# Kernel optimization log

Measured on AMD Instinct MI355X. Metric: run time of the kernel, lower is better.

The kernel has to match this reference:

```python
import jax, jax.numpy as jnp
import numpy as np

B, S, D, H, HD = 2, 2048, 2048, 16, 128  # batch, seq, embed, heads, head_dim


def setup_inputs() -> dict:
    key = jax.random.key(0)
    k0, k1, k2 = jax.random.split(key, 3)
    hidden_states = jax.random.normal(k0, (B, S, D), dtype=jnp.float32)
    # fused QKV projection: [D, H*HD + 2*HD] (multi-query: single shared K and V head)
    W_attn = jax.random.normal(k1, (D, H * HD + 2 * HD), dtype=jnp.float32) * 0.02
    b_attn = jnp.zeros((H * HD + 2 * HD,), dtype=jnp.float32)
    W_proj = jax.random.normal(k2, (D, D), dtype=jnp.float32) * 0.02
    b_proj = jnp.zeros((D,), dtype=jnp.float32)
    # causal mask, broadcastable to (B, Q, H, K); True = attend
    attention_mask = jnp.tril(jnp.ones((S, S), dtype=bool))[None, :, None, :]
    return {
        "hidden_states": hidden_states,
        "W_attn": W_attn,
        "b_attn": b_attn,
        "W_proj": W_proj,
        "b_proj": b_proj,
        "attention_mask": attention_mask,
    }


def reference(hidden_states, W_attn, b_attn, W_proj, b_proj, attention_mask):
    # fused QKV, then split into Q (H heads) and shared K/V (multi-query)
    qkv = hidden_states @ W_attn + b_attn          # (B, S, H*HD + 2*HD)
    q = qkv[..., : H * HD].reshape(B, S, H, HD)    # (B, Q, H, hd)
    key_t = qkv[..., H * HD : H * HD + HD]         # (B, K, hd) shared K head
    value = qkv[..., H * HD + HD :]                # (B, K, hd) shared V head

    # dtype == softmax_dtype (fp32) -> upcast=False, unscale=1
    scale_factor = 1.0 / (HD ** 0.5)               # scale_attn_weights
    attn_weights = jnp.einsum("bqhd,bkd->bqhk", q, key_t) * scale_factor
    mask_value = jnp.finfo(jnp.float32).min
    attn_weights = jnp.where(attention_mask, attn_weights, mask_value)
    attn_weights = jax.nn.softmax(attn_weights, axis=-1)

    attn_output = jnp.einsum("bqhk,bkd->bqhd", attn_weights, value)
    attn_output = attn_output.reshape(B, S, H * HD)
    return attn_output @ W_proj + b_proj           # (B, S, D)
```

## Files before the change

### kernel.cpp

```cpp
#include <hip/hip_runtime.h>
#include <math.h>

constexpr int cB  = 2;
constexpr int cS  = 2048;
constexpr int cD  = 2048;
constexpr int cH  = 16;
constexpr int cHD = 128;
constexpr int cNQKV = cH * cHD + 2 * cHD;

typedef __attribute__((ext_vector_type(8))) short bf16x8;
typedef __attribute__((ext_vector_type(4))) float f32x4;

__device__ __forceinline__ short f2bf(float f) {
    union { float f; unsigned u; } v; v.f = f;
    unsigned r = (v.u + 0x7FFFu + ((v.u >> 16) & 1u)) >> 16;
    return (short)r;
}

typedef __attribute__((address_space(3))) void lds_t;
typedef const __attribute__((address_space(1))) void gbl_t;
__device__ __forceinline__ void gld16(const void* g, void* l) {
    __builtin_amdgcn_global_load_lds((gbl_t*)g, (lds_t*)l, 16, 0, 0);
}

__global__ __launch_bounds__(256) void conv_bf16(
    const float* __restrict__ src, short* __restrict__ dst)
{
    size_t i = ((size_t)blockIdx.x * 256 + threadIdx.x) * 8;
    float4 a = *(const float4*)(src + i);
    float4 b = *(const float4*)(src + i + 4);
    bf16x8 o;
    o[0] = f2bf(a.x); o[1] = f2bf(a.y); o[2] = f2bf(a.z); o[3] = f2bf(a.w);
    o[4] = f2bf(b.x); o[5] = f2bf(b.y); o[6] = f2bf(b.z); o[7] = f2bf(b.w);
    *(bf16x8*)(dst + i) = o;
}

__global__ __launch_bounds__(256) void transpose_bf16(
    const float* __restrict__ src, short* __restrict__ dst, int K, int N)
{
    __shared__ short t[32][33];
    const int n0 = blockIdx.x * 32, k0 = blockIdx.y * 32;
    const int x = threadIdx.x & 31, y = threadIdx.x >> 5;
#pragma unroll
    for (int i = 0; i < 4; ++i)
        t[y + 8 * i][x] = f2bf(src[(size_t)(k0 + y + 8 * i) * N + n0 + x]);
    __syncthreads();
#pragma unroll
    for (int i = 0; i < 4; ++i)
        dst[(size_t)(n0 + y + 8 * i) * K + k0 + x] = t[x][y + 8 * i];
}

template<bool BF16_OUT>
__global__ __launch_bounds__(256) void gemm_mfma(
    const short* __restrict__ A, const short* __restrict__ Bt,
    const float* __restrict__ bias, void* __restrict__ Cout,
    int M, int N, int K, float qscale, int qcols)
{
    __shared__ short As[128 * 32];
    __shared__ short Bs[128 * 32];

    const int tid = threadIdx.x;
    const int lane = tid & 63, n16 = lane & 15, quad = lane >> 4;
    const int wave = tid >> 6, wm = wave >> 1, wn = wave & 1;
    const int m0 = blockIdx.y * 128, n0 = blockIdx.x * 128;

    f32x4 acc[4][4];
#pragma unroll
    for (int i = 0; i < 4; ++i)
#pragma unroll
        for (int j = 0; j < 4; ++j) acc[i][j] = 0.0f;

    const int s0 = tid, s1 = tid + 256;
    const short* Ag0 = A  + (size_t)(m0 + (s0 >> 2)) * K + (s0 & 3) * 8;
    const short* Ag1 = A  + (size_t)(m0 + (s1 >> 2)) * K + (s1 & 3) * 8;
    const short* Bg0 = Bt + (size_t)(n0 + (s0 >> 2)) * K + (s0 & 3) * 8;
    const short* Bg1 = Bt + (size_t)(n0 + (s1 >> 2)) * K + (s1 & 3) * 8;

    for (int k0 = 0; k0 < K; k0 += 32) {
        gld16(Ag0 + k0, &As[s0 * 8]);
        gld16(Ag1 + k0, &As[s1 * 8]);
        gld16(Bg0 + k0, &Bs[s0 * 8]);
        gld16(Bg1 + k0, &Bs[s1 * 8]);
        __syncthreads();
        bf16x8 af[4], bfr[4];
#pragma unroll
        for (int mt = 0; mt < 4; ++mt)
            af[mt] = *(const bf16x8*)&As[(wm * 64 + mt * 16 + n16) * 32 + quad * 8];
#pragma unroll
        for (int nt = 0; nt < 4; ++nt)
            bfr[nt] = *(const bf16x8*)&Bs[(wn * 64 + nt * 16 + n16) * 32 + quad * 8];
#pragma unroll
        for (int mt = 0; mt < 4; ++mt)
#pragma unroll
            for (int nt = 0; nt < 4; ++nt)
                acc[mt][nt] = __builtin_amdgcn_mfma_f32_16x16x32_bf16(
                    af[mt], bfr[nt], acc[mt][nt], 0, 0, 0);
        __syncthreads();
    }

#pragma unroll
    for (int nt = 0; nt < 4; ++nt) {
        const int col = n0 + wn * 64 + nt * 16 + n16;
        const float bv = bias[col];
        const float sc = (col < qcols) ? qscale : 1.0f;
#pragma unroll
        for (int mt = 0; mt < 4; ++mt)
#pragma unroll
            for (int r = 0; r < 4; ++r) {
                const int row = m0 + wm * 64 + mt * 16 + quad * 4 + r;
                const float v = (acc[mt][nt][r] + bv) * sc;
                if (BF16_OUT) ((short*)Cout)[(size_t)row * N + col] = f2bf(v);
                else          ((float*)Cout)[(size_t)row * N + col] = v;
            }
    }
}

__global__ __launch_bounds__(256) void prep_v(
    const short* __restrict__ qkvb, short* __restrict__ Vt)
{
    const int b  = blockIdx.y;
    const int k0 = blockIdx.x * 64;
    const int t  = threadIdx.x;
#pragma unroll
    for (int i = 0; i < 32; ++i) {
        int idx = i * 256 + t;
        int hd = idx >> 6, key = idx & 63;
        Vt[((size_t)b * cHD + hd) * cS + k0 + key] =
            qkvb[((size_t)(b * cS + k0 + key)) * cNQKV + cH * cHD + cHD + hd];
    }
}

__global__ __launch_bounds__(256) void attn_mfma(
    const short* __restrict__ qkvb, const short* __restrict__ Vt,
    short* __restrict__ out)
{
    const int tid  = threadIdx.x;
    const int wave = tid >> 6;
    const int lane = tid & 63;
    const int n16  = lane & 15;
    const int quad = lane >> 4;
    const int h  = blockIdx.y;
    const int b  = blockIdx.z;

    __shared__ __align__(16) short Ks[2][8192];
    __shared__ __align__(16) short Vs[2][8192];
    __shared__ __align__(16) short Ps[4][16][72];

    const int part = lane & 3;
    const int krow = lane >> 2;

    const short* kglob = qkvb + (size_t)b * cS * cNQKV + cH * cHD;
    const short* vbase = Vt + (size_t)b * cHD * cS;

    int cur = 0;

    auto stage = [&](int buf, int k0) {
        const short* kr = kglob + (size_t)(k0 + wave * 16 + krow) * cNQKV + part * 8;
#pragma unroll
        for (int j = 0; j < 4; ++j)
            gld16(kr + j * 32, &Ks[buf][(j * 4 + wave) * 512]);
#pragma unroll
        for (int j = 0; j < 4; ++j) {
            const int idx = j * 4 + wave;
            const int c2 = idx >> 3;
            const int hd = (idx & 7) * 16 + krow;
            gld16(vbase + (size_t)hd * cS + k0 + c2 * 32 + part * 8,
                  &Vs[buf][idx * 512]);
        }
    };

#pragma unroll 1
    for (int seg = 0; seg < 2; ++seg) {
        const int qt = seg ? (int)blockIdx.x : 31 - (int)blockIdx.x;
        const int q0 = qt * 64 + wave * 16;
        const int nkt = qt + 1;

        bf16x8 qf[4];
        {
            const short* qbase = qkvb + ((size_t)(b * cS) + q0 + n16) * cNQKV
                               + h * cHD + quad * 8;
#pragma unroll
            for (int ch = 0; ch < 4; ++ch) qf[ch] = *(const bf16x8*)(qbase + ch * 32);
        }

        f32x4 oc[8];
#pragma unroll
        for (int on = 0; on < 8; ++on) oc[on] = 0.0f;
        float lp[4] = {0.0f, 0.0f, 0.0f, 0.0f};

        __syncthreads();
        stage(cur, 0);

#pragma unroll 1
        for (int kt = 0; kt < nkt; ++kt) {
            const int k0 = kt * 64;
            __syncthreads();
            if (kt + 1 < nkt) stage(cur ^ 1, k0 + 64);

            f32x4 sc[4];
#pragma unroll
            for (int nt = 0; nt < 4; ++nt) sc[nt] = 0.0f;
            __builtin_amdgcn_s_setprio(1);
#pragma unroll
            for (int nt = 0; nt < 4; ++nt) {
#pragma unroll
                for (int ch = 0; ch < 4; ++ch) {
                    bf16x8 kf = *(const bf16x8*)&Ks[cur][(ch * 64 + nt * 16 + n16) * 32 + quad * 8];
                    sc[nt] = __builtin_amdgcn_mfma_f32_16x16x32_bf16(qf[ch], kf, sc[nt], 0, 0, 0);
                }
            }
            __builtin_amdgcn_s_setprio(0);

            if (kt == nkt - 1) {
#pragma unroll
                for (int nt = 0; nt < 4; ++nt)
#pragma unroll
                    for (int r = 0; r < 4; ++r) {
                        int row = q0 + quad * 4 + r;
                        int col = k0 + nt * 16 + n16;
                        if (col > row) sc[nt][r] = -1e30f;
                    }
            }

#pragma unroll
            for (int r = 0; r < 4; ++r)
#pragma unroll
                for (int nt = 0; nt < 4; ++nt) {
                    float p = __expf(sc[nt][r]);
                    lp[r] += p;
                    Ps[wave][quad * 4 + r][nt * 16 + n16] = f2bf(p);
                }

            bf16x8 pf0 = *(const bf16x8*)&Ps[wave][n16][quad * 8];
            bf16x8 pf1 = *(const bf16x8*)&Ps[wave][n16][32 + quad * 8];

            __builtin_amdgcn_s_setprio(1);
#pragma unroll
            for (int on = 0; on < 8; ++on) {
                bf16x8 vf0 = *(const bf16x8*)&Vs[cur][(on * 16 + n16) * 32 + quad * 8];
                bf16x8 vf1 = *(const bf16x8*)&Vs[cur][(128 * 32) + (on * 16 + n16) * 32 + quad * 8];
                oc[on] = __builtin_amdgcn_mfma_f32_16x16x32_bf16(pf0, vf0, oc[on], 0, 0, 0);
                oc[on] = __builtin_amdgcn_mfma_f32_16x16x32_bf16(pf1, vf1, oc[on], 0, 0, 0);
            }
            __builtin_amdgcn_s_setprio(0);

            cur ^= 1;
        }

        float inv[4];
#pragma unroll
        for (int r = 0; r < 4; ++r) {
            float t = lp[r];
            t += __shfl_xor(t, 1);
            t += __shfl_xor(t, 2);
            t += __shfl_xor(t, 4);
            t += __shfl_xor(t, 8);
            inv[r] = 1.0f / t;
        }
        short* obase = out + ((size_t)(b * cS) + q0) * cD + h * cHD;
#pragma unroll
        for (int on = 0; on < 8; ++on)
#pragma unroll
            for (int r = 0; r < 4; ++r)
                obase[(size_t)(quad * 4 + r) * cD + on * 16 + n16] = f2bf(oc[on][r] * inv[r]);
    }
}

extern "C" void kernel_launch(void* const* d_in, const int* in_sizes, int n_in,
                              void* d_out, int out_size, void* d_ws, size_t ws_size,
                              hipStream_t stream)
{
    const float* hidden = (const float*)d_in[0];
    const float* W_attn = (const float*)d_in[1];
    const float* b_attn = (const float*)d_in[2];
    const float* W_proj = (const float*)d_in[3];
    const float* b_proj = (const float*)d_in[4];
    float* out = (float*)d_out;

    const int M = cB * cS;
    short* qkvb = (short*)d_ws;
    short* Ah   = qkvb + (size_t)M * cNQKV;
    short* Wb   = Ah   + (size_t)M * cD;
    short* Wpb  = Wb   + (size_t)cNQKV * cD;
    short* Vt   = Wpb  + (size_t)cD * cD;
    short* attno = Ah;

    const float scale = 0.088388347648318447f;

    conv_bf16<<<(size_t)M * cD / 2048, 256, 0, stream>>>(hidden, Ah);
    transpose_bf16<<<dim3(cNQKV / 32, cD / 32), 256, 0, stream>>>(W_attn, Wb, cD, cNQKV);
    transpose_bf16<<<dim3(cD / 32, cD / 32), 256, 0, stream>>>(W_proj, Wpb, cD, cD);

    gemm_mfma<true><<<dim3(cNQKV / 128, M / 128), 256, 0, stream>>>(
        Ah, Wb, b_attn, qkvb, M, cNQKV, cD, scale, cH * cHD);

    prep_v<<<dim3(cS / 64, cB), 256, 0, stream>>>(qkvb, Vt);

    attn_mfma<<<dim3(cS / 128, cH, cB), 256, 0, stream>>>(qkvb, Vt, attno);

    gemm_mfma<false><<<dim3(cD / 128, M / 128), 256, 0, stream>>>(
        attno, Wpb, b_proj, out, M, cD, cD, 1.0f, 0);
}
```

Before: 323.9 us.

## Switch attention to 32x32x16 MFMA with register-resident P and swizzled LDS

Rewrites the attention kernel to use 32x32x16 bf16 MFMA tiles, with 2 waves of 32 query rows each instead of 4 waves of 16. The computed S^T fragment is kept in registers and turned into the P operand through packed bf16 conversion and cross-half lane shuffles, which removes the LDS round trip for P. K and V tiles are staged into LDS with an XOR swizzle to avoid bank conflicts. The trade-off is higher register pressure from 16-wide accumulators and half as many waves per block, which may reduce occupancy or latency hiding.

New measurement: 346.9 us. 1.07x slower.

```diff
diff --git a/kernel.cpp b/kernel.cpp
--- a/kernel.cpp
+++ b/kernel.cpp
@@ -10,11 +10,17 @@
 
 typedef __attribute__((ext_vector_type(8))) short bf16x8;
 typedef __attribute__((ext_vector_type(4))) float f32x4;
+typedef __attribute__((ext_vector_type(16))) float f32x16;
 
 __device__ __forceinline__ short f2bf(float f) {
     union { float f; unsigned u; } v; v.f = f;
     unsigned r = (v.u + 0x7FFFu + ((v.u >> 16) & 1u)) >> 16;
     return (short)r;
+}
+
+__device__ __forceinline__ unsigned pk_bf16(float lo, float hi_) {
+    return (unsigned)(unsigned short)f2bf(lo)
+         | ((unsigned)(unsigned short)f2bf(hi_) << 16);
 }
 
 typedef __attribute__((address_space(3))) void lds_t;
@@ -130,63 +136,69 @@
     }
 }
 
-__global__ __launch_bounds__(256) void attn_mfma(
+__global__ __launch_bounds__(128) void attn_mfma(
     const short* __restrict__ qkvb, const short* __restrict__ Vt,
     short* __restrict__ out)
 {
     const int tid  = threadIdx.x;
     const int wave = tid >> 6;
     const int lane = tid & 63;
-    const int n16  = lane & 15;
-    const int quad = lane >> 4;
+    const int q32  = lane & 31;
+    const int hi   = lane >> 5;
     const int h  = blockIdx.y;
     const int b  = blockIdx.z;
 
-    __shared__ __align__(16) short Ks[2][8192];
-    __shared__ __align__(16) short Vs[2][8192];
-    __shared__ __align__(16) short Ps[4][16][72];
-
-    const int part = lane & 3;
-    const int krow = lane >> 2;
+    __shared__ __align__(16) short Ks[2][64 * 128];
+    __shared__ __align__(16) short Vs[2][128 * 64];
+    __shared__ __align__(16) float Linv[2][32];
 
     const short* kglob = qkvb + (size_t)b * cS * cNQKV + cH * cHD;
     const short* vbase = Vt + (size_t)b * cHD * cS;
 
+    const int kl = lane >> 4;
+    const int kx = (lane & 15) * 16;
+    const int vdl = lane >> 3;
+    const int vx  = (lane & 7) * 16;
+
     int cur = 0;
 
     auto stage = [&](int buf, int k0) {
-        const short* kr = kglob + (size_t)(k0 + wave * 16 + krow) * cNQKV + part * 8;
-#pragma unroll
-        for (int j = 0; j < 4; ++j)
-            gld16(kr + j * 32, &Ks[buf][(j * 4 + wave) * 512]);
-#pragma unroll
-        for (int j = 0; j < 4; ++j) {
-            const int idx = j * 4 + wave;
-            const int c2 = idx >> 3;
-            const int hd = (idx & 7) * 16 + krow;
-            gld16(vbase + (size_t)hd * cS + k0 + c2 * 32 + part * 8,
-                  &Vs[buf][idx * 512]);
+#pragma unroll
+        for (int j = 0; j < 8; ++j) {
+            const int keyt = (wave * 8 + j) * 4 + kl;
+            const int srcb = kx ^ ((keyt & 15) << 4);
+            gld16((const char*)(kglob + (size_t)(k0 + keyt) * cNQKV) + srcb,
+                  &Ks[buf][(wave * 8 + j) * 512]);
+        }
+#pragma unroll
+        for (int j = 0; j < 8; ++j) {
+            const int d = (wave * 8 + j) * 8 + vdl;
+            const int srcb = vx ^ ((d & 7) << 4);
+            gld16((const char*)(vbase + (size_t)d * cS + k0) + srcb,
+                  &Vs[buf][(wave * 8 + j) * 512]);
         }
     };
 
 #pragma unroll 1
     for (int seg = 0; seg < 2; ++seg) {
         const int qt = seg ? (int)blockIdx.x : 31 - (int)blockIdx.x;
-        const int q0 = qt * 64 + wave * 16;
+        const int qb = qt * 64;
+        const int qg = qb + wave * 32 + q32;
         const int nkt = qt + 1;
 
-        bf16x8 qf[4];
+        bf16x8 qf[8];
         {
-            const short* qbase = qkvb + ((size_t)(b * cS) + q0 + n16) * cNQKV
-                               + h * cHD + quad * 8;
-#pragma unroll
-            for (int ch = 0; ch < 4; ++ch) qf[ch] = *(const bf16x8*)(qbase + ch * 32);
+            const short* qbase = qkvb + ((size_t)(b * cS) + qg) * cNQKV
+                               + h * cHD + hi * 8;
+#pragma unroll
+            for (int dblk = 0; dblk < 8; ++dblk)
+                qf[dblk] = *(const bf16x8*)(qbase + dblk * 16);
         }
 
-        f32x4 oc[8];
-#pragma unroll
-        for (int on = 0; on < 8; ++on) oc[on] = 0.0f;
-        float lp[4] = {0.0f, 0.0f, 0.0f, 0.0f};
+        f32x16 oc[4];
+#pragma unroll
+        for (int i = 0; i < 4; ++i) oc[i] = 0.0f;
+        float lp = 0.0f;
 
         __syncthreads();
         stage(cur, 0);
@@ -197,72 +209,93 @@
             __syncthreads();
             if (kt + 1 < nkt) stage(cur ^ 1, k0 + 64);
 
-            f32x4 sc[4];
-#pragma unroll
-            for (int nt = 0; nt < 4; ++nt) sc[nt] = 0.0f;
+            f32x16 sc[2];
+            sc[0] = 0.0f; sc[1] = 0.0f;
             __builtin_amdgcn_s_setprio(1);
 #pragma unroll
-            for (int nt = 0; nt < 4; ++nt) {
-#pragma unroll
-                for (int ch = 0; ch < 4; ++ch) {
-                    bf16x8 kf = *(const bf16x8*)&Ks[cur][(ch * 64 + nt * 16 + n16) * 32 + quad * 8];
-                    sc[nt] = __builtin_amdgcn_mfma_f32_16x16x32_bf16(qf[ch], kf, sc[nt], 0, 0, 0);
+            for (int kt2 = 0; kt2 < 2; ++kt2) {
+                const int key = kt2 * 32 + q32;
+                const char* krow = (const char*)&Ks[cur][key * 128];
+                const int swz = (key & 15) << 4;
+#pragma unroll
+                for (int dblk = 0; dblk < 8; ++dblk) {
+                    bf16x8 kf = *(const bf16x8*)(krow + ((dblk * 32 + hi * 16) ^ swz));
+                    sc[kt2] = __builtin_amdgcn_mfma_f32_32x32x16_bf16(
+                        kf, qf[dblk], sc[kt2], 0, 0, 0);
                 }
             }
             __builtin_amdgcn_s_setprio(0);
 
-            if (kt == nkt - 1) {
-#pragma unroll
-                for (int nt = 0; nt < 4; ++nt)
-#pragma unroll
-                    for (int r = 0; r < 4; ++r) {
-                        int row = q0 + quad * 4 + r;
-                        int col = k0 + nt * 16 + n16;
-                        if (col > row) sc[nt][r] = -1e30f;
+            const bool diag = (kt == nkt - 1);
+            float e[2][16];
+#pragma unroll
+            for (int kt2 = 0; kt2 < 2; ++kt2)
+#pragma unroll
+                for (int r = 0; r < 16; ++r) {
+                    float s = sc[kt2][r];
+                    if (diag) {
+                        int kgl = k0 + kt2 * 32 + (r & 3) + 8 * (r >> 2) + 4 * hi;
+                        if (kgl > qg) s = -1e30f;
                     }
+                    float p = __expf(s);
+                    lp += p;
+                    e[kt2][r] = p;
+                }
+
+            bf16x8 pa[4];
+#pragma unroll
+            for (int kblk = 0; kblk < 4; ++kblk) {
+                const int kt2 = kblk >> 1;
+                const int rb  = 8 * (kblk & 1);
+                unsigned wA0 = pk_bf16(e[kt2][rb + 0], e[kt2][rb + 1]);
+                unsigned wA1 = pk_bf16(e[kt2][rb + 2], e[kt2][rb + 3]);
+                unsigned wB0 = pk_bf16(e[kt2][rb + 4], e[kt2][rb + 5]);
+                unsigned wB1 = pk_bf16(e[kt2][rb + 6], e[kt2][rb + 7]);
+                unsigned keep0 = hi ? wB0 : wA0, keep1 = hi ? wB1 : wA1;
+                unsigned send0 = hi ? wA0 : wB0, send1 = hi ? wA1 : wB1;
+                unsigned recv0 = (unsigned)__shfl_xor((int)send0, 32);
+                unsigned recv1 = (unsigned)__shfl_xor((int)send1, 32);
+                union { unsigned u[4]; bf16x8 v; } uu;
+                uu.u[0] = hi ? recv0 : keep0;
+                uu.u[1] = hi ? recv1 : keep1;
+                uu.u[2] = hi ? keep0 : recv0;
+                uu.u[3] = hi ? keep1 : recv1;
+                pa[kblk] = uu.v;
             }
 
-#pragma unroll
-            for (int r = 0; r < 4; ++r)
-#pragma unroll
-                for (int nt = 0; nt < 4; ++nt) {
-                    float p = __expf(sc[nt][r]);
-                    lp[r] += p;
-                    Ps[wave][quad * 4 + r][nt * 16 + n16] = f2bf(p);
+            __builtin_amdgcn_s_setprio(1);
+#pragma unroll
+            for (int kblk = 0; kblk < 4; ++kblk)
+#pragma unroll
+                for (int dtile = 0; dtile < 4; ++dtile) {
+                    const int d = dtile * 32 + q32;
+                    const char* vrow = (const char*)&Vs[cur][d * 64];
+                    bf16x8 vf = *(const bf16x8*)(vrow + ((kblk * 32 + hi * 16) ^ ((d & 7) << 4)));
+                    oc[dtile] = __builtin_amdgcn_mfma_f32_32x32x16_bf16(
+                        pa[kblk], vf, oc[dtile], 0, 0, 0);
                 }
-
-            bf16x8 pf0 = *(const bf16x8*)&Ps[wave][n16][quad * 8];
-            bf16x8 pf1 = *(const bf16x8*)&Ps[wave][n16][32 + quad * 8];
-
-            __builtin_amdgcn_s_setprio(1);
-#pragma unroll
-            for (int on = 0; on < 8; ++on) {
-                bf16x8 vf0 = *(const bf16x8*)&Vs[cur][(on * 16 + n16) * 32 + quad * 8];
-                bf16x8 vf1 = *(const bf16x8*)&Vs[cur][(128 * 32) + (on * 16 + n16) * 32 + quad * 8];
-                oc[on] = __builtin_amdgcn_mfma_f32_16x16x32_bf16(pf0, vf0, oc[on], 0, 0, 0);
-                oc[on] = __builtin_amdgcn_mfma_f32_16x16x32_bf16(pf1, vf1, oc[on], 0, 0, 0);
-            }
             __builtin_amdgcn_s_setprio(0);
 
             cur ^= 1;
         }
 
-        float inv[4];
-#pragma unroll
-        for (int r = 0; r < 4; ++r) {
-            float t = lp[r];
-            t += __shfl_xor(t, 1);
-            t += __shfl_xor(t, 2);
-            t += __shfl_xor(t, 4);
-            t += __shfl_xor(t, 8);
-            inv[r] = 1.0f / t;
-        }
-        short* obase = out + ((size_t)(b * cS) + q0) * cD + h * cHD;
-#pragma unroll
-        for (int on = 0; on < 8; ++on)
-#pragma unroll
-            for (int r = 0; r < 4; ++r)
-                obase[(size_t)(quad * 4 + r) * cD + on * 16 + n16] = f2bf(oc[on][r] * inv[r]);
+        lp += __shfl_xor(lp, 32);
+        if (hi == 0) Linv[wave][q32] = 1.0f / lp;
+        __syncthreads();
+        f32x4 invv[4];
+#pragma unroll
+        for (int g = 0; g < 4; ++g)
+            invv[g] = *(const f32x4*)&Linv[wave][g * 8 + hi * 4];
+
+        short* obase = out + ((size_t)(b * cS) + qb + wave * 32) * cD + h * cHD;
+#pragma unroll
+        for (int dtile = 0; dtile < 4; ++dtile)
+#pragma unroll
+            for (int r = 0; r < 16; ++r) {
+                const int q = (r & 3) + 8 * (r >> 2) + 4 * hi;
+                obase[(size_t)q * cD + dtile * 32 + q32] =
+                    f2bf(oc[dtile][r] * invv[r >> 2][r & 3]);
+            }
     }
 }
 
@@ -296,7 +329,7 @@
 
     prep_v<<<dim3(cS / 64, cB), 256, 0, stream>>>(qkvb, Vt);
 
-    attn_mfma<<<dim3(cS / 128, cH, cB), 256, 0, stream>>>(qkvb, Vt, attno);
+    attn_mfma<<<dim3(16, cH, cB), 128, 0, stream>>>(qkvb, Vt, attno);
 
     gemm_mfma<false><<<dim3(cD / 128, M / 128), 256, 0, stream>>>(
         attno, Wpb, b_proj, out, M, cD, cD, 1.0f, 0);
```
